# Kernel optimization log

Hardware: AMD Instinct MI355X
Metric: run time of the kernel (lower is better)

## Reference

```python
import jax, jax.numpy as jnp
import numpy as np

LN_EPS = 1e-5

def _ln(x):
    # haiku LayerNorm([-1], create_scale=False, create_offset=False)
    mu = x.mean(axis=-1, keepdims=True)
    var = x.var(axis=-1, keepdims=True)
    return (x - mu) * jax.lax.rsqrt(var + LN_EPS)

def setup_inputs() -> dict:
    key = jax.random.key(0)
    ks = jax.random.split(key, 10)
    N, L, P = 512, 256, 64
    inp = {
        "local": jax.random.normal(ks[0], (N, L), jnp.float32),
        "pair": jax.random.normal(ks[1], (N, N, P), jnp.float32),
        "mask": jax.random.randint(ks[2], (N,), 0, 2, jnp.int32),
        "W_pair_gate": jax.random.normal(ks[3], (P, 2 * P), jnp.float32) / np.sqrt(P),
        "W_pair_value": jax.random.normal(ks[4], (P, 2 * P), jnp.float32) / np.sqrt(P),
        "W_left_gate": jax.random.normal(ks[5], (L, 2 * P), jnp.float32) / np.sqrt(L),
        "W_left_value": jax.random.normal(ks[6], (L, 2 * P), jnp.float32) / np.sqrt(L),
        "W_right_gate": jax.random.normal(ks[7], (L, 2 * P), jnp.float32) / np.sqrt(L),
        "W_right_value": jax.random.normal(ks[8], (L, 2 * P), jnp.float32) / np.sqrt(L),
        "W_out": jax.random.normal(ks[9], (3 * P, P), jnp.float32) / np.sqrt(3 * P),
    }
    return inp

def reference(local, pair, mask, W_pair_gate, W_pair_value, W_left_gate,
              W_left_value, W_right_gate, W_right_value, W_out):
    maskb = mask.astype(bool)
    pair_mask = maskb[:, None] & maskb[None, :]                  # (N, N)
    l = _ln(local)                                               # (N, L)
    p = _ln(pair)                                                # (N, N, P)
    pair_gate = p @ W_pair_gate                                  # (N, N, 2P)
    pair_value = p @ W_pair_value                                # (N, N, 2P)
    # left: broadcast local over axis 0/1, gelu-gate, mask, reduce over j
    left_gate = jax.nn.gelu((l @ W_left_gate)[:, None] + pair_gate)
    left_value = (l @ W_left_value)[None, :] + pair_value
    left = jnp.where(pair_mask[..., None], left_gate * left_value, 0).sum(axis=1)  # (N, 2P)
    right_gate = jax.nn.gelu((l @ W_right_gate)[None, :] + pair_gate)
    right_value = (l @ W_right_value)[:, None] + pair_value
    right = jnp.where(pair_mask[..., None], right_gate * right_value, 0).sum(axis=0)  # (N, 2P)
    paired_pseudo_local = _ln(left[:, None] + right[None, :])    # (N, N, 2P)
    pair_hidden = jnp.concatenate((p, paired_pseudo_local), axis=-1)  # (N, N, 3P)
    return pair_hidden @ W_out                                   # (N, N, P)
```

## Files before the change

kernel.cpp:

```cpp
#include <hip/hip_runtime.h>
#include <math.h>

#define LN_EPS 1e-5f


typedef __bf16 bf16x8 __attribute__((ext_vector_type(8)));
typedef float f32x16 __attribute__((ext_vector_type(16)));

__device__ __forceinline__ float gelu_f(float x) {
    float x2 = x * x;
    float e = __builtin_amdgcn_exp2f(x * fmaf(0.10294423f, x2, 2.3022079f));
    float r = __builtin_amdgcn_rcpf(e + 1.0f);
    return fmaf(-x, r, x);
}

__global__ __launch_bounds__(256) void kA(
    const float* __restrict__ loc,
    const float* __restrict__ Wlg, const float* __restrict__ Wlv,
    const float* __restrict__ Wrg, const float* __restrict__ Wrv,
    float* __restrict__ proj, const int* __restrict__ mask,
    int* __restrict__ act, float* __restrict__ left, float* __restrict__ right) {
    const int t = threadIdx.x;
    if (blockIdx.x == 64) {
        if (blockIdx.y == 1) {
            float4 z = {0.f, 0.f, 0.f, 0.f};
            for (int idx = t; idx < 16384; idx += 256) ((float4*)left)[idx] = z;
        } else if (blockIdx.y == 2) {
            float4 z = {0.f, 0.f, 0.f, 0.f};
            for (int idx = t; idx < 16384; idx += 256) ((float4*)right)[idx] = z;
        } else if (blockIdx.y == 0) {
            __shared__ int cnt_sh[8];
            const int lane = t & 63, wv = t >> 6;
            int msave[2];
            unsigned long long bsave[2];
#pragma unroll
            for (int ch = 0; ch < 2; ++ch) {
                int m = (mask[ch * 256 + t] != 0);
                unsigned long long b = __ballot(m);
                if (lane == 0) cnt_sh[ch * 4 + wv] = __popcll(b);
                msave[ch] = m;
                bsave[ch] = b;
            }
            __syncthreads();
#pragma unroll
            for (int ch = 0; ch < 2; ++ch) {
                int base = 0;
                for (int u = 0; u < ch * 4 + wv; ++u) base += cnt_sh[u];
                int pos = base + __popcll(bsave[ch] & ((1ull << lane) - 1ull));
                if (msave[ch]) act[1 + pos] = ch * 256 + t;
            }
            if (t == 0) {
                int ctot = 0;
                for (int u = 0; u < 8; ++u) ctot += cnt_sh[u];
                act[0] = ctot;
            }
        }
        return;
    }
    __shared__ float ln_sh[8][260];
    __shared__ float red_sh[128][9];
    const int i0 = blockIdx.x * 8;
    const int mat = blockIdx.y;
    const float* __restrict__ W = (mat == 0) ? Wlg : (mat == 1) ? Wlv
                                 : (mat == 2) ? Wrg : Wrv;
    {
        int row = t >> 5, l32 = t & 31;
        const float4* src = (const float4*)(loc + (i0 + row) * 256);
        float4 v0 = src[l32 * 2];
        float4 v1 = src[l32 * 2 + 1];
        float s = (v0.x + v0.y) + (v0.z + v0.w) + (v1.x + v1.y) + (v1.z + v1.w);
        float ss = v0.x * v0.x + v0.y * v0.y + v0.z * v0.z + v0.w * v0.w +
                   v1.x * v1.x + v1.y * v1.y + v1.z * v1.z + v1.w * v1.w;
#pragma unroll
        for (int off = 1; off < 32; off <<= 1) {
            s += __shfl_xor(s, off);
            ss += __shfl_xor(ss, off);
        }
        float mu = s * (1.f / 256.f);
        float rs = rsqrtf(ss * (1.f / 256.f) - mu * mu + LN_EPS);
        float4 o0, o1;
        o0.x = (v0.x - mu) * rs; o0.y = (v0.y - mu) * rs;
        o0.z = (v0.z - mu) * rs; o0.w = (v0.w - mu) * rs;
        o1.x = (v1.x - mu) * rs; o1.y = (v1.y - mu) * rs;
        o1.z = (v1.z - mu) * rs; o1.w = (v1.w - mu) * rs;
        *(float4*)&ln_sh[row][l32 * 8] = o0;
        *(float4*)&ln_sh[row][l32 * 8 + 4] = o1;
    }
    __syncthreads();

    const int n = t & 127;
    const int kh = t >> 7;
    float acc[8] = {0.f, 0.f, 0.f, 0.f, 0.f, 0.f, 0.f, 0.f};
#pragma unroll 2
    for (int c = 0; c < 32; ++c) {
        const int kc = kh * 128 + c * 4;
        float w0 = W[(kc + 0) * 128 + n];
        float w1 = W[(kc + 1) * 128 + n];
        float w2 = W[(kc + 2) * 128 + n];
        float w3 = W[(kc + 3) * 128 + n];
#pragma unroll
        for (int r = 0; r < 8; ++r) {
            float4 l4 = *(const float4*)&ln_sh[r][kc];
            acc[r] += l4.x * w0 + l4.y * w1 + l4.z * w2 + l4.w * w3;
        }
    }
    if (kh == 1) {
#pragma unroll
        for (int r = 0; r < 8; ++r) red_sh[n][r] = acc[r];
    }
    __syncthreads();
    if (kh == 0) {
#pragma unroll
        for (int r = 0; r < 8; ++r)
            proj[mat * 65536 + (i0 + r) * 128 + n] = acc[r] + red_sh[n][r];
    }
}

#define KB_TI 2
__global__ __launch_bounds__(256) void kB(
    const float* __restrict__ pair, const int* __restrict__ act,
    const float* __restrict__ Wg, const float* __restrict__ Wv,
    const float* __restrict__ lg, const float* __restrict__ lv,
    const float* __restrict__ rg, const float* __restrict__ rv,
    float* __restrict__ left, float* __restrict__ right) {
    __shared__ __bf16 A_sh[2][32][72];
    __shared__ int ji_sh[32];
    __shared__ int ii_sh[KB_TI];

    const int cnt = act[0];
    const int j0 = blockIdx.x * 32;
    const int ibase = blockIdx.y * KB_TI;
    if (j0 >= cnt || ibase >= cnt) return;
    const int nact = min(KB_TI, cnt - ibase);

    const int t = threadIdx.x;
    const int lane = t & 63;
    const int w = t >> 6;
    const int c = lane & 31;
    const int half = lane >> 5;
    const int n = w * 32 + c;

    if (t < 32) ji_sh[t] = act[1 + min(j0 + t, cnt - 1)];
    if (t >= 64 && t < 64 + KB_TI) ii_sh[t - 64] = act[1 + min(ibase + (t - 64), cnt - 1)];
    __syncthreads();

    bf16x8 bg[4], bv[4];
#pragma unroll
    for (int kt = 0; kt < 4; ++kt) {
        bf16x8 vg, vv;
#pragma unroll
        for (int e = 0; e < 8; ++e) {
            int kr = kt * 16 + half * 8 + e;
            vg[e] = (__bf16)Wg[kr * 128 + n];
            vv[e] = (__bf16)Wv[kr * 128 + n];
        }
        bg[kt] = vg; bv[kt] = vv;
    }

    float lvr[16], rgr[16];
    unsigned jmask = 0;
#pragma unroll
    for (int r = 0; r < 16; ++r) {
        int m = 4 * half + (r & 3) + 8 * (r >> 2);
        int j = ji_sh[m];
        lvr[r] = lv[j * 128 + n];
        rgr[r] = rg[j * 128 + n];
        if (j0 + m < cnt) jmask |= (1u << r);
    }

    const int srow = t >> 3;
    const int kseg = (t & 7) * 8;
    float4 p0, p1;
    float plg, prv;
    {
        int iF = ii_sh[0];
        const float* src = pair + ((size_t)iF * 512 + ji_sh[srow]) * 64 + kseg;
        p0 = *(const float4*)src;
        p1 = *(const float4*)(src + 4);
        plg = lg[iF * 128 + n];
        prv = rv[iF * 128 + n];
    }

    auto lnwrite = [&](int buf) {
        float s = (p0.x + p0.y) + (p0.z + p0.w) + (p1.x + p1.y) + (p1.z + p1.w);
        float ss = p0.x * p0.x + p0.y * p0.y + p0.z * p0.z + p0.w * p0.w +
                   p1.x * p1.x + p1.y * p1.y + p1.z * p1.z + p1.w * p1.w;
        s += __shfl_xor(s, 1); ss += __shfl_xor(ss, 1);
        s += __shfl_xor(s, 2); ss += __shfl_xor(ss, 2);
        s += __shfl_xor(s, 4); ss += __shfl_xor(ss, 4);
        float mu = s * (1.f / 64.f);
        float rs = rsqrtf(ss * (1.f / 64.f) - mu * mu + LN_EPS);
        bf16x8 o;
        o[0] = (__bf16)((p0.x - mu) * rs); o[1] = (__bf16)((p0.y - mu) * rs);
        o[2] = (__bf16)((p0.z - mu) * rs); o[3] = (__bf16)((p0.w - mu) * rs);
        o[4] = (__bf16)((p1.x - mu) * rs); o[5] = (__bf16)((p1.y - mu) * rs);
        o[6] = (__bf16)((p1.z - mu) * rs); o[7] = (__bf16)((p1.w - mu) * rs);
        *(bf16x8*)&A_sh[buf][srow][kseg] = o;
    };
    lnwrite(0);
    __syncthreads();

    float racc[16];
#pragma unroll
    for (int r = 0; r < 16; ++r) racc[r] = 0.f;

    for (int ii = 0; ii < nact; ++ii) {
        const int i = ii_sh[ii];
        const float lgi = plg;
        const float rvi = prv;
        if (ii + 1 < nact) {
            int iF = ii_sh[ii + 1];
            const float* src = pair + ((size_t)iF * 512 + ji_sh[srow]) * 64 + kseg;
            p0 = *(const float4*)src;
            p1 = *(const float4*)(src + 4);
            plg = lg[iF * 128 + n];
            prv = rv[iF * 128 + n];
        }

        f32x16 ag = {}; f32x16 av = {};
#pragma unroll
        for (int kt = 0; kt < 4; ++kt) {
            bf16x8 af = *(const bf16x8*)&A_sh[ii & 1][c][kt * 16 + half * 8];
            ag = __builtin_amdgcn_mfma_f32_32x32x16_bf16(af, bg[kt], ag, 0, 0, 0);
            av = __builtin_amdgcn_mfma_f32_32x32x16_bf16(af, bv[kt], av, 0, 0, 0);
        }

        float lsum = 0.f;
#pragma unroll
        for (int r = 0; r < 16; ++r) {
            float pg = ag[r], pv = av[r];
            float lres = gelu_f(lgi + pg) * (lvr[r] + pv);
            float rres = gelu_f(rgr[r] + pg) * (rvi + pv);
            lsum += ((jmask >> r) & 1) ? lres : 0.f;
            racc[r] += rres;
        }
        float tot = lsum + __shfl_xor(lsum, 32);
        if (lane < 32) atomicAdd(&left[i * 128 + n], tot);

        if (ii + 1 < nact) lnwrite((ii + 1) & 1);
        __syncthreads();
    }

#pragma unroll
    for (int r = 0; r < 16; ++r) {
        if ((jmask >> r) & 1) {
            int m = 4 * half + (r & 3) + 8 * (r >> 2);
            atomicAdd(&right[ji_sh[m] * 128 + n], racc[r]);
        }
    }
}

__global__ __launch_bounds__(256) void kD(
    const float* __restrict__ left, const float* __restrict__ right,
    const float* __restrict__ W_out,
    float* __restrict__ Aw, float* __restrict__ Bw,
    float* __restrict__ rsrm, float* __restrict__ cs) {
    const int bx = blockIdx.x;
    const int t = threadIdx.x;
    if (bx < 256) {
        __shared__ float l_sh[32][68];
        __shared__ float r_sh[32][68];
        const int tx = t & 15, ty = t >> 4;
        const int i0 = (bx & 15) * 32, j0 = (bx >> 4) * 32;
        float acc00 = 0.f, acc01 = 0.f, acc10 = 0.f, acc11 = 0.f;
        float sL0 = 0.f, ssL0 = 0.f, sL1 = 0.f, ssL1 = 0.f;
        float sR0 = 0.f, ssR0 = 0.f, sR1 = 0.f, ssR1 = 0.f;
        for (int kc = 0; kc < 128; kc += 64) {
            __syncthreads();
#pragma unroll
            for (int u = 0; u < 2; ++u) {
                int fi = t + u * 256;
                int row = fi >> 4, kq = (fi & 15) * 4;
                float4 lv4 = *(const float4*)(left + (i0 + row) * 128 + kc + kq);
                float4 rv4 = *(const float4*)(right + (j0 + row) * 128 + kc + kq);
                *(float4*)&l_sh[row][kq] = lv4;
                *(float4*)&r_sh[row][kq] = rv4;
            }
            __syncthreads();
#pragma unroll
            for (int k4 = 0; k4 < 64; k4 += 4) {
                float4 l0 = *(const float4*)&l_sh[ty * 2 + 0][k4];
                float4 l1 = *(const float4*)&l_sh[ty * 2 + 1][k4];
                float4 r0 = *(const float4*)&r_sh[tx * 2 + 0][k4];
                float4 r1 = *(const float4*)&r_sh[tx * 2 + 1][k4];
                acc00 += l0.x * r0.x + l0.y * r0.y + l0.z * r0.z + l0.w * r0.w;
                acc01 += l0.x * r1.x + l0.y * r1.y + l0.z * r1.z + l0.w * r1.w;
                acc10 += l1.x * r0.x + l1.y * r0.y + l1.z * r0.z + l1.w * r0.w;
                acc11 += l1.x * r1.x + l1.y * r1.y + l1.z * r1.z + l1.w * r1.w;
                sL0 += (l0.x + l0.y) + (l0.z + l0.w);
                ssL0 += l0.x * l0.x + l0.y * l0.y + l0.z * l0.z + l0.w * l0.w;
                sL1 += (l1.x + l1.y) + (l1.z + l1.w);
                ssL1 += l1.x * l1.x + l1.y * l1.y + l1.z * l1.z + l1.w * l1.w;
                sR0 += (r0.x + r0.y) + (r0.z + r0.w);
                ssR0 += r0.x * r0.x + r0.y * r0.y + r0.z * r0.z + r0.w * r0.w;
                sR1 += (r1.x + r1.y) + (r1.z + r1.w);
                ssR1 += r1.x * r1.x + r1.y * r1.y + r1.z * r1.z + r1.w * r1.w;
            }
        }
        {
            float sLa[2] = {sL0, sL1}, ssLa[2] = {ssL0, ssL1};
            float sRb[2] = {sR0, sR1}, ssRb[2] = {ssR0, ssR1};
            float accv[2][2] = {{acc00, acc01}, {acc10, acc11}};
#pragma unroll
            for (int a = 0; a < 2; ++a) {
#pragma unroll
                for (int b = 0; b < 2; ++b) {
                    float mu = (sLa[a] + sRb[b]) * (1.f / 128.f);
                    float var = fmaf(-mu, mu,
                                     (ssLa[a] + 2.f * accv[a][b] + ssRb[b]) * (1.f / 128.f));
                    float rs = rsqrtf(var + LN_EPS);
                    size_t idx = (size_t)(i0 + ty * 2 + a) * 512 + (j0 + tx * 2 + b);
                    float2 v; v.x = rs; v.y = rs * mu;
                    ((float2*)rsrm)[idx] = v;
                }
            }
        }
    } else {
        const int id = bx - 256;
        const int which = id >> 8;
        const int sub = t >> 7;
        const int tt = t & 127;
        const int r = (id & 255) * 2 + sub;
        const float* src = which ? right : left;
        __shared__ float row_sh[2][128];
        row_sh[sub][tt] = src[r * 128 + tt];
        __syncthreads();
        if (tt < 64) {
            float a = 0.f;
            const float* W2 = W_out + 64 * 64;
#pragma unroll 8
            for (int m = 0; m < 128; ++m) a += row_sh[sub][m] * W2[m * 64 + tt];
            (which ? Bw : Aw)[r * 64 + tt] = a;
        }
        if (id == 0 && t < 64) {
            float c0 = 0.f, c1 = 0.f;
            for (int k = 0; k < 64; ++k) c0 += W_out[k * 64 + t];
            for (int m = 0; m < 128; ++m) c1 += W_out[(64 + m) * 64 + t];
            cs[t] = c0;
            cs[64 + t] = c1;
        }
    }
}

__global__ __launch_bounds__(256) void kC(
    const float* __restrict__ pair, const float* __restrict__ Wout,
    const float* __restrict__ Aw, const float* __restrict__ Bw,
    const float* __restrict__ rsrm,
    const float* __restrict__ cs, float* __restrict__ out) {
    const int t = threadIdx.x;
    const int lane = t & 63;
    const int w = t >> 6;
    const int c = lane & 31;
    const int half = lane >> 5;
    const int i0 = blockIdx.x * 4;
    const int j0 = blockIdx.y * 64;
    const int mt = w & 1;
    const int nt = w >> 1;
    const int n = nt * 32 + c;
    const int jrow = j0 + mt * 32 + c;

    const float* __restrict__ abase = pair + ((size_t)i0 * 512 + jrow) * 64 + half * 8;

    float4 va[8], vb[8];
#pragma unroll
    for (int kt = 0; kt < 4; ++kt) {
        va[2 * kt] = *(const float4*)(abase + kt * 16);
        va[2 * kt + 1] = *(const float4*)(abase + kt * 16 + 4);
    }

    bf16x8 bo[4];
#pragma unroll
    for (int kt = 0; kt < 4; ++kt) {
        bf16x8 bb;
#pragma unroll
        for (int e = 0; e < 8; ++e)
            bb[e] = (__bf16)Wout[(kt * 16 + half * 8 + e) * 64 + n];
        bo[kt] = bb;
    }
    float Bv[16];
#pragma unroll
    for (int r = 0; r < 16; ++r) {
        int jp = j0 + mt * 32 + 4 * half + (r & 3) + 8 * (r >> 2);
        Bv[r] = Bw[jp * 64 + n];
    }
    const float cs1n = cs[64 + n];

    auto stats = [&](float4 (&buf)[8], float& rs_o, float& nmr_o) {
        float s = 0.f, ss = 0.f;
#pragma unroll
        for (int u = 0; u < 8; ++u) {
            s += (buf[u].x + buf[u].y) + (buf[u].z + buf[u].w);
            ss += buf[u].x * buf[u].x + buf[u].y * buf[u].y +
                  buf[u].z * buf[u].z + buf[u].w * buf[u].w;
        }
        s += __shfl_xor(s, 32);
        ss += __shfl_xor(ss, 32);
        float mu = s * (1.f / 64.f);
        float rs = rsqrtf(ss * (1.f / 64.f) - mu * mu + LN_EPS);
        rs_o = rs;
        nmr_o = -mu * rs;
    };

    float rsA, nmrA, rsB, nmrB;
    stats(va, rsA, nmrA);

    auto body = [&](float4 (&cur)[8], float4 (&nxt)[8], int ii,
                    float rs_c, float nmr_c, float& rs_n, float& nmr_n) {
        if (ii < 3) {
            const float* src = abase + (size_t)(ii + 1) * 512 * 64;
#pragma unroll
            for (int kt = 0; kt < 4; ++kt) {
                nxt[2 * kt] = *(const float4*)(src + kt * 16);
                nxt[2 * kt + 1] = *(const float4*)(src + kt * 16 + 4);
            }
        }
        const int i = i0 + ii;
        const float A_in = Aw[i * 64 + n];

        f32x16 acc = {};
#pragma unroll
        for (int kt = 0; kt < 4; ++kt) {
            bf16x8 af;
#pragma unroll
            for (int u = 0; u < 2; ++u) {
                float4 vv = cur[2 * kt + u];
                af[u * 4 + 0] = (__bf16)fmaf(vv.x, rs_c, nmr_c);
                af[u * 4 + 1] = (__bf16)fmaf(vv.y, rs_c, nmr_c);
                af[u * 4 + 2] = (__bf16)fmaf(vv.z, rs_c, nmr_c);
                af[u * 4 + 3] = (__bf16)fmaf(vv.w, rs_c, nmr_c);
            }
            acc = __builtin_amdgcn_mfma_f32_32x32x16_bf16(af, bo[kt], acc, 0, 0, 0);
        }

        if (ii < 3) stats(nxt, rs_n, nmr_n);

#pragma unroll
        for (int r = 0; r < 16; ++r) {
            int jp = j0 + mt * 32 + 4 * half + (r & 3) + 8 * (r >> 2);
            size_t idx = (size_t)i * 512 + jp;
            float2 rr = ((const float2*)rsrm)[idx];
            out[idx * 64 + n] =
                fmaf(rr.x, A_in + Bv[r], fmaf(-rr.y, cs1n, acc[r]));
        }
    };
    body(va, vb, 0, rsA, nmrA, rsB, nmrB);
    body(vb, va, 1, rsB, nmrB, rsA, nmrA);
    body(va, vb, 2, rsA, nmrA, rsB, nmrB);
    body(vb, va, 3, rsB, nmrB, rsA, nmrA);
}

extern "C" void kernel_launch(void* const* d_in, const int* in_sizes, int n_in,
                              void* d_out, int out_size, void* d_ws, size_t ws_size,
                              hipStream_t stream) {
    const float* loc  = (const float*)d_in[0];
    const float* pair = (const float*)d_in[1];
    const int*   mask = (const int*)d_in[2];
    const float* Wpg  = (const float*)d_in[3];
    const float* Wpv  = (const float*)d_in[4];
    const float* Wlg  = (const float*)d_in[5];
    const float* Wlv  = (const float*)d_in[6];
    const float* Wrg  = (const float*)d_in[7];
    const float* Wrv  = (const float*)d_in[8];
    const float* Wout = (const float*)d_in[9];
    float* out = (float*)d_out;
    float* ws = (float*)d_ws;

    float* proj   = ws;
    float* left   = ws + 262144;
    float* right  = ws + 327680;
    float* Aw     = ws + 393216;
    float* Bw     = ws + 425984;
    float* rsrm   = ws + 458752;
    float* cs     = ws + 983040;
    int*   act    = (int*)(ws + 983168);

    kA<<<dim3(65, 4), 256, 0, stream>>>(loc, Wlg, Wlv, Wrg, Wrv, proj,
                                        mask, act, left, right);
    kB<<<dim3(16, 256), 256, 0, stream>>>(pair, act, Wpg, Wpv,
                                          proj, proj + 65536, proj + 131072,
                                          proj + 196608, left, right);
    kD<<<768, 256, 0, stream>>>(left, right, Wout, Aw, Bw, rsrm, cs);
    kC<<<dim3(128, 8), 256, 0, stream>>>(pair, Wout, Aw, Bw, rsrm, cs, out);
}
```

Before: 204.1 us.

## Fuse pseudo-local LayerNorm stats into output kernel, drop rsrm buffer

Moves the per-(i,j) LayerNorm statistics of left[i]+right[j] out of kD and into kC. kC now stages a 64-row tile of right and four rows of left in shared memory and computes the stats per block into shared memory. This removes the rsrm workspace round-trip (2 MB write plus read) and 256 kD blocks. The cost is extra shared memory and two barriers in kC, plus recomputing right-row loads across the 128 i-blocks.

```diff
diff --git a/kernel.cpp b/kernel.cpp
--- a/kernel.cpp
+++ b/kernel.cpp
@@ -253,100 +253,41 @@
 __global__ __launch_bounds__(256) void kD(
     const float* __restrict__ left, const float* __restrict__ right,
     const float* __restrict__ W_out,
-    float* __restrict__ Aw, float* __restrict__ Bw,
-    float* __restrict__ rsrm, float* __restrict__ cs) {
-    const int bx = blockIdx.x;
+    float* __restrict__ Aw, float* __restrict__ Bw, float* __restrict__ cs) {
+    const int id = blockIdx.x;
     const int t = threadIdx.x;
-    if (bx < 256) {
-        __shared__ float l_sh[32][68];
-        __shared__ float r_sh[32][68];
-        const int tx = t & 15, ty = t >> 4;
-        const int i0 = (bx & 15) * 32, j0 = (bx >> 4) * 32;
-        float acc00 = 0.f, acc01 = 0.f, acc10 = 0.f, acc11 = 0.f;
-        float sL0 = 0.f, ssL0 = 0.f, sL1 = 0.f, ssL1 = 0.f;
-        float sR0 = 0.f, ssR0 = 0.f, sR1 = 0.f, ssR1 = 0.f;
-        for (int kc = 0; kc < 128; kc += 64) {
-            __syncthreads();
-#pragma unroll
-            for (int u = 0; u < 2; ++u) {
-                int fi = t + u * 256;
-                int row = fi >> 4, kq = (fi & 15) * 4;
-                float4 lv4 = *(const float4*)(left + (i0 + row) * 128 + kc + kq);
-                float4 rv4 = *(const float4*)(right + (j0 + row) * 128 + kc + kq);
-                *(float4*)&l_sh[row][kq] = lv4;
-                *(float4*)&r_sh[row][kq] = rv4;
-            }
-            __syncthreads();
-#pragma unroll
-            for (int k4 = 0; k4 < 64; k4 += 4) {
-                float4 l0 = *(const float4*)&l_sh[ty * 2 + 0][k4];
-                float4 l1 = *(const float4*)&l_sh[ty * 2 + 1][k4];
-                float4 r0 = *(const float4*)&r_sh[tx * 2 + 0][k4];
-                float4 r1 = *(const float4*)&r_sh[tx * 2 + 1][k4];
-                acc00 += l0.x * r0.x + l0.y * r0.y + l0.z * r0.z + l0.w * r0.w;
-                acc01 += l0.x * r1.x + l0.y * r1.y + l0.z * r1.z + l0.w * r1.w;
-                acc10 += l1.x * r0.x + l1.y * r0.y + l1.z * r0.z + l1.w * r0.w;
-                acc11 += l1.x * r1.x + l1.y * r1.y + l1.z * r1.z + l1.w * r1.w;
-                sL0 += (l0.x + l0.y) + (l0.z + l0.w);
-                ssL0 += l0.x * l0.x + l0.y * l0.y + l0.z * l0.z + l0.w * l0.w;
-                sL1 += (l1.x + l1.y) + (l1.z + l1.w);
-                ssL1 += l1.x * l1.x + l1.y * l1.y + l1.z * l1.z + l1.w * l1.w;
-                sR0 += (r0.x + r0.y) + (r0.z + r0.w);
-                ssR0 += r0.x * r0.x + r0.y * r0.y + r0.z * r0.z + r0.w * r0.w;
-                sR1 += (r1.x + r1.y) + (r1.z + r1.w);
-                ssR1 += r1.x * r1.x + r1.y * r1.y + r1.z * r1.z + r1.w * r1.w;
-            }
-        }
-        {
-            float sLa[2] = {sL0, sL1}, ssLa[2] = {ssL0, ssL1};
-            float sRb[2] = {sR0, sR1}, ssRb[2] = {ssR0, ssR1};
-            float accv[2][2] = {{acc00, acc01}, {acc10, acc11}};
-#pragma unroll
-            for (int a = 0; a < 2; ++a) {
-#pragma unroll
-                for (int b = 0; b < 2; ++b) {
-                    float mu = (sLa[a] + sRb[b]) * (1.f / 128.f);
-                    float var = fmaf(-mu, mu,
-                                     (ssLa[a] + 2.f * accv[a][b] + ssRb[b]) * (1.f / 128.f));
-                    float rs = rsqrtf(var + LN_EPS);
-                    size_t idx = (size_t)(i0 + ty * 2 + a) * 512 + (j0 + tx * 2 + b);
-                    float2 v; v.x = rs; v.y = rs * mu;
-                    ((float2*)rsrm)[idx] = v;
-                }
-            }
-        }
-    } else {
-        const int id = bx - 256;
-        const int which = id >> 8;
-        const int sub = t >> 7;
-        const int tt = t & 127;
-        const int r = (id & 255) * 2 + sub;
-        const float* src = which ? right : left;
-        __shared__ float row_sh[2][128];
-        row_sh[sub][tt] = src[r * 128 + tt];
-        __syncthreads();
-        if (tt < 64) {
-            float a = 0.f;
-            const float* W2 = W_out + 64 * 64;
+    const int which = id >> 8;
+    const int sub = t >> 7;
+    const int tt = t & 127;
+    const int r = (id & 255) * 2 + sub;
+    const float* src = which ? right : left;
+    __shared__ float row_sh[2][128];
+    row_sh[sub][tt] = src[r * 128 + tt];
+    __syncthreads();
+    if (tt < 64) {
+        float a = 0.f;
+        const float* W2 = W_out + 64 * 64;
 #pragma unroll 8
-            for (int m = 0; m < 128; ++m) a += row_sh[sub][m] * W2[m * 64 + tt];
-            (which ? Bw : Aw)[r * 64 + tt] = a;
-        }
-        if (id == 0 && t < 64) {
-            float c0 = 0.f, c1 = 0.f;
-            for (int k = 0; k < 64; ++k) c0 += W_out[k * 64 + t];
-            for (int m = 0; m < 128; ++m) c1 += W_out[(64 + m) * 64 + t];
-            cs[t] = c0;
-            cs[64 + t] = c1;
-        }
+        for (int m = 0; m < 128; ++m) a += row_sh[sub][m] * W2[m * 64 + tt];
+        (which ? Bw : Aw)[r * 64 + tt] = a;
+    }
+    if (id == 0 && t < 64) {
+        float c0 = 0.f, c1 = 0.f;
+        for (int k = 0; k < 64; ++k) c0 += W_out[k * 64 + t];
+        for (int m = 0; m < 128; ++m) c1 += W_out[(64 + m) * 64 + t];
+        cs[t] = c0;
+        cs[64 + t] = c1;
     }
 }
 
 __global__ __launch_bounds__(256) void kC(
     const float* __restrict__ pair, const float* __restrict__ Wout,
     const float* __restrict__ Aw, const float* __restrict__ Bw,
-    const float* __restrict__ rsrm,
+    const float* __restrict__ left, const float* __restrict__ right,
     const float* __restrict__ cs, float* __restrict__ out) {
+    __shared__ float l_sh[4][132];
+    __shared__ float r_sh[64][132];
+    __shared__ float2 rsrm_sh[4][64];
     const int t = threadIdx.x;
     const int lane = t & 63;
     const int w = t >> 6;
@@ -368,6 +309,25 @@
         va[2 * kt + 1] = *(const float4*)(abase + kt * 16 + 4);
     }
 
+    {
+        int rr = t >> 2, ch = (t & 3) * 32;
+        const float4* src = (const float4*)(right + (j0 + rr) * 128 + ch);
+        float4 tmp[8];
+#pragma unroll
+        for (int m = 0; m < 8; ++m) tmp[m] = src[m];
+#pragma unroll
+        for (int m = 0; m < 8; ++m) *(float4*)&r_sh[rr][ch + 4 * m] = tmp[m];
+        if (t < 32) {
+            int li = t >> 3, lc = (t & 7) * 16;
+            const float4* ls = (const float4*)(left + (i0 + li) * 128 + lc);
+            float4 lt[4];
+#pragma unroll
+            for (int m = 0; m < 4; ++m) lt[m] = ls[m];
+#pragma unroll
+            for (int m = 0; m < 4; ++m) *(float4*)&l_sh[li][lc + 4 * m] = lt[m];
+        }
+    }
+
     bf16x8 bo[4];
 #pragma unroll
     for (int kt = 0; kt < 4; ++kt) {
@@ -384,6 +344,27 @@
         Bv[r] = Bw[jp * 64 + n];
     }
     const float cs1n = cs[64 + n];
+
+    __syncthreads();
+
+    {
+        float acc = 0.f, sL = 0.f, ssL = 0.f, sR = 0.f, ssR = 0.f;
+#pragma unroll 8
+        for (int k4 = 0; k4 < 128; k4 += 4) {
+            float4 l4 = *(const float4*)&l_sh[w][k4];
+            float4 r4 = *(const float4*)&r_sh[lane][k4];
+            acc += l4.x * r4.x + l4.y * r4.y + l4.z * r4.z + l4.w * r4.w;
+            sL += (l4.x + l4.y) + (l4.z + l4.w);
+            ssL += l4.x * l4.x + l4.y * l4.y + l4.z * l4.z + l4.w * l4.w;
+            sR += (r4.x + r4.y) + (r4.z + r4.w);
+            ssR += r4.x * r4.x + r4.y * r4.y + r4.z * r4.z + r4.w * r4.w;
+        }
+        float mu = (sL + sR) * (1.f / 128.f);
+        float var = fmaf(-mu, mu, (ssL + 2.f * acc + ssR) * (1.f / 128.f));
+        float rs = rsqrtf(var + LN_EPS);
+        float2 v; v.x = rs; v.y = rs * mu;
+        rsrm_sh[w][lane] = v;
+    }
 
     auto stats = [&](float4 (&buf)[8], float& rs_o, float& nmr_o) {
         float s = 0.f, ss = 0.f;
@@ -403,6 +384,7 @@
 
     float rsA, nmrA, rsB, nmrB;
     stats(va, rsA, nmrA);
+    __syncthreads();
 
     auto body = [&](float4 (&cur)[8], float4 (&nxt)[8], int ii,
                     float rs_c, float nmr_c, float& rs_n, float& nmr_n) {
@@ -436,10 +418,9 @@
 
 #pragma unroll
         for (int r = 0; r < 16; ++r) {
-            int jp = j0 + mt * 32 + 4 * half + (r & 3) + 8 * (r >> 2);
-            size_t idx = (size_t)i * 512 + jp;
-            float2 rr = ((const float2*)rsrm)[idx];
-            out[idx * 64 + n] =
+            int jl = mt * 32 + 4 * half + (r & 3) + 8 * (r >> 2);
+            float2 rr = rsrm_sh[ii][jl];
+            out[((size_t)i * 512 + j0 + jl) * 64 + n] =
                 fmaf(rr.x, A_in + Bv[r], fmaf(-rr.y, cs1n, acc[r]));
         }
     };
@@ -470,7 +451,6 @@
     float* right  = ws + 327680;
     float* Aw     = ws + 393216;
     float* Bw     = ws + 425984;
-    float* rsrm   = ws + 458752;
     float* cs     = ws + 983040;
     int*   act    = (int*)(ws + 983168);
 
@@ -479,6 +459,6 @@
     kB<<<dim3(16, 256), 256, 0, stream>>>(pair, act, Wpg, Wpv,
                                           proj, proj + 65536, proj + 131072,
                                           proj + 196608, left, right);
-    kD<<<768, 256, 0, stream>>>(left, right, Wout, Aw, Bw, rsrm, cs);
-    kC<<<dim3(128, 8), 256, 0, stream>>>(pair, Wout, Aw, Bw, rsrm, cs, out);
-}
+    kD<<<512, 256, 0, stream>>>(left, right, Wout, Aw, Bw, cs);
+    kC<<<dim3(128, 8), 256, 0, stream>>>(pair, Wout, Aw, Bw, left, right, cs, out);
+}
```

New measurement: 208.7 us. 1.02x slower.
